# Kernel optimization log

Measured on AMD Instinct MI355X. Metric: run time of the kernel, lower is better.

## Reference

```python
import jax, jax.numpy as jnp
import numpy as np

MAX_DELAY = 128
INPUT = 64
HIDDEN = 128
HALF = HIDDEN // 2
OUT = 64
B = 32
T = 128
OUT_LEN = 64


def setup_inputs() -> dict:
    key = jax.random.key(0)
    ks = jax.random.split(key, 10)
    w = lambda k, sh: (jax.random.normal(k, sh, jnp.float32) * 0.05)
    return {
        "x": jax.random.normal(ks[0], (B, T, INPUT), jnp.float32),
        "lengths": jax.random.randint(ks[1], (B,), 0, T, jnp.int32),
        "out_lengths": OUT_LEN,
        "Wm": w(ks[2], (INPUT + HIDDEN, HIDDEN)), "bm": jnp.zeros((HIDDEN,), jnp.float32),
        "W1": w(ks[3], (HIDDEN, HALF)), "b1": jnp.zeros((HALF,), jnp.float32),
        "W2": w(ks[4], (HALF, 2 * HIDDEN)), "b2": jnp.zeros((2 * HIDDEN,), jnp.float32),
        "Wo": w(ks[5], (HIDDEN, OUT)), "bo": jnp.zeros((OUT,), jnp.float32),
    }


def reference(x, lengths, out_lengths, Wm, bm, W1, b1, W2, b2, Wo, bo):
    # index_tensor: (1, 1, max_delay) in [0, 1)
    index = (jnp.arange(MAX_DELAY, dtype=x.dtype) / MAX_DELAY)[None, None, :]

    def tau_gen(msg):  # msg: (B, H)
        h = jax.nn.relu(msg @ W1 + b1)
        tg = jax.nn.sigmoid(h @ W2 + b2)  # (B, 2H)
        return tg[:, :HIDDEN], tg[:, HIDDEN:]

    def update_buffer(buffer, msg, tau, mem_i):
        # shift left, zero-pad at the end
        new_buf = jnp.pad(buffer[:, :, 1:], ((0, 0), (0, 0), (0, 1)))
        iw = mem_i[..., None] * (1.0 - jnp.abs(tau[..., None] - index)) ** 2  # (B,H,D)
        return (1.0 - iw) * new_buf + iw * msg[..., None]

    masks = (jnp.arange(T) < lengths[:, None]).astype(x.dtype)  # (B, T)

    def enc_step(buffer, inp):
        x_t, mask = inp  # (B, I), (B,)
        m = mask[:, None]  # (B, 1)
        msg = m * jnp.tanh(jnp.concatenate([x_t, buffer[:, :, 0]], axis=-1) @ Wm + bm)
        tau, mem_i = tau_gen(msg)
        new_buf = update_buffer(buffer, msg, tau, mem_i)
        buffer = jnp.where(m[..., None] > 0, new_buf, buffer)
        return buffer, None

    buffer0 = jnp.zeros((B, HIDDEN, MAX_DELAY), x.dtype)
    buffer, _ = jax.lax.scan(enc_step, buffer0, (x.transpose(1, 0, 2), masks.T))

    x0 = jnp.zeros((B, INPUT), x.dtype)

    def dec_step(buffer, _):
        msg = jnp.tanh(jnp.concatenate([x0, buffer[:, :, 0]], axis=-1) @ Wm + bm)
        tau, mem_i = tau_gen(msg)
        buffer = update_buffer(buffer, msg, tau, mem_i)
        return buffer, msg @ Wo + bo

    _, outs = jax.lax.scan(dec_step, buffer, None, length=out_lengths)
    return outs.transpose(1, 0, 2)  # (B, out_lengths, OUT)
```

## Files before the change

kernel.cpp:

```cpp
#include <hip/hip_runtime.h>
#include <math.h>

typedef __attribute__((ext_vector_type(2))) float f32x2;

#define MAX_DELAY 128
#define INPUT 64
#define HIDDEN 128
#define HALF 64
#define OUT 64
#define BATCH 32
#define T 128
#define OUT_LEN 64
#define NTHR 512

static __device__ __forceinline__ f32x2 splat2(float v) { f32x2 r; r.x = v; r.y = v; return r; }

template <int CTRL>
static __device__ __forceinline__ float dpp_movf(float v) {
    return __int_as_float(__builtin_amdgcn_update_dpp(
        0, __float_as_int(v), CTRL, 0xF, 0xF, true));
}
#define DPP_XOR1 0xB1
#define DPP_XOR2 0x4E
#define DPP_ROT1 0x39
#define DPP_MIR8 0x141

__global__ __launch_bounds__(NTHR, 2)
void delayrnn_kernel(
    const float* __restrict__ x,
    const int*   __restrict__ lengths,
    const float* __restrict__ Wm,
    const float* __restrict__ bm,
    const float* __restrict__ W1,
    const float* __restrict__ b1,
    const float* __restrict__ W2,
    const float* __restrict__ b2,
    const float* __restrict__ Wo,
    const float* __restrict__ bo,
    float* __restrict__ out)
{
    const int b   = blockIdx.x;
    const int tid = threadIdx.x;
    const int len = lengths[b];
    const int total = len + OUT_LEN;

    const int h  = tid >> 2, q  = tid & 3;
    const int qq = q & 1,    qh = q >> 1;
    const int k1 = tid >> 3, r1 = tid & 7;
    const int co = tid >> 3, ro = tid & 7;

    f32x2 wm2[24];
#pragma unroll
    for (int j = 0; j < 24; ++j) {
        wm2[j].x = Wm[(q * 48 + 2 * j)     * HIDDEN + h];
        wm2[j].y = Wm[(q * 48 + 2 * j + 1) * HIDDEN + h];
    }
    f32x2 w12[8];
#pragma unroll
    for (int j = 0; j < 8; ++j) {
        w12[j].x = W1[(r1 * 16 + 2 * j)     * HALF + k1];
        w12[j].y = W1[(r1 * 16 + 2 * j + 1) * HALF + k1];
    }
    const int c2 = h + 128 * qh;
    f32x2 w22[16];
#pragma unroll
    for (int j = 0; j < 16; ++j) {
        w22[j].x = W2[(qq * 32 + 2 * j)     * (2 * HIDDEN) + c2];
        w22[j].y = W2[(qq * 32 + 2 * j + 1) * (2 * HIDDEN) + c2];
    }
    f32x2 wo2[8];
#pragma unroll
    for (int j = 0; j < 8; ++j) {
        wo2[j].x = Wo[(ro * 16 + 2 * j)     * OUT + co];
        wo2[j].y = Wo[(ro * 16 + 2 * j + 1) * OUT + co];
    }
    const float bm_r = bm[h];
    const float b1_r = b1[k1];
    const float b2_r = b2[c2];
    const float bo_r = bo[co];

    float buf[32];
#pragma unroll
    for (int d = 0; d < 32; ++d) buf[d] = 0.f;

    __shared__ float s_x[T * INPUT];
    __shared__ float s_v[INPUT + HIDDEN];
    __shared__ float s_msg[HIDDEN];
    __shared__ float s_h1[HALF];

    for (int idx = tid; idx < T * INPUT; idx += NTHR)
        s_x[idx] = x[b * T * INPUT + idx];
    if (tid < INPUT) s_v[tid] = (0 < len) ? x[b * T * INPUT + tid] : 0.f;
    if (tid >= INPUT && tid < INPUT + HIDDEN) s_v[tid] = 0.f;
    __syncthreads();

    const float ivb = (float)q * 0.25f;

    for (int i = 0; i < total; ++i) {
        const f32x2* v2 = (const f32x2*)(s_v + q * 48);
        f32x2 a0 = splat2(0.f), a1 = splat2(0.f), a2 = splat2(0.f), a3 = splat2(0.f);
#pragma unroll
        for (int j = 0; j < 24; j += 4) {
            a0 += wm2[j] * v2[j];         a1 += wm2[j + 1] * v2[j + 1];
            a2 += wm2[j + 2] * v2[j + 2]; a3 += wm2[j + 3] * v2[j + 3];
        }
        f32x2 aa = (a0 + a1) + (a2 + a3);
        float p = aa.x + aa.y;
        p += dpp_movf<DPP_XOR1>(p);
        p += dpp_movf<DPP_XOR2>(p);
        const float z  = p + bm_r;
        const float e2 = __expf(2.f * z);
        const float msg = 1.f - 2.f * __builtin_amdgcn_rcpf(e2 + 1.f);
        if (q == 0) s_msg[h] = msg;
        __syncthreads();

        const f32x2* m2 = (const f32x2*)(s_msg + r1 * 16);
        f32x2 c0 = splat2(0.f), c1 = splat2(0.f);
#pragma unroll
        for (int j = 0; j < 8; j += 2) { c0 += w12[j] * m2[j]; c1 += w12[j + 1] * m2[j + 1]; }
        f32x2 cc = c0 + c1;
        float p1 = cc.x + cc.y;
        p1 += dpp_movf<DPP_XOR1>(p1);
        p1 += dpp_movf<DPP_XOR2>(p1);
        p1 += dpp_movf<DPP_MIR8>(p1);
        if (r1 == 0) s_h1[k1] = fmaxf(p1 + b1_r, 0.f);
        __syncthreads();

        const f32x2* h2 = (const f32x2*)(s_h1 + qq * 32);
        f32x2 t0 = splat2(0.f), t1 = splat2(0.f);
#pragma unroll
        for (int j = 0; j < 16; j += 2) { t0 += w22[j] * h2[j]; t1 += w22[j + 1] * h2[j + 1]; }
        f32x2 tt = t0 + t1;
        float pt = tt.x + tt.y;
        pt += dpp_movf<DPP_XOR1>(pt);
        const float own = __builtin_amdgcn_rcpf(1.f + __expf(-(pt + b2_r)));
        const float oth = dpp_movf<DPP_XOR2>(own);
        const float tau_r = qh ? oth : own;
        const float mem_r = qh ? own : oth;

        {
            float tail_in = dpp_movf<DPP_ROT1>(buf[0]);
            if (q == 3) tail_in = 0.f;
            const float taup = tau_r - ivb;
            const f32x2 tau2 = splat2(taup);
            const f32x2 mem2 = splat2(mem_r);
            const f32x2 m2m  = splat2(-2.f * mem_r);
            const f32x2 msg2 = splat2(msg);
#pragma unroll
            for (int mp = 0; mp < 16; ++mp) {
                const int d = 2 * mp;
                f32x2 nb;
                nb.x = buf[d + 1];
                nb.y = (mp < 15) ? buf[d + 2] : tail_in;
                f32x2 t;
                t.x = tau2.x - (float)d       * (1.f / MAX_DELAY);
                t.y = tau2.y - (float)(d + 1) * (1.f / MAX_DELAY);
                f32x2 a  = __builtin_elementwise_max(t, -t);
                f32x2 f1 = a * mem2 + m2m;
                f32x2 iw = a * f1 + mem2;
                f32x2 dd = msg2 - nb;
                f32x2 nv = iw * dd + nb;
                buf[d] = nv.x; buf[d + 1] = nv.y;
            }
        }
        if (q == 0) s_v[INPUT + h] = buf[0];

        if (i >= len) {
            const f32x2* mo2 = (const f32x2*)(s_msg + ro * 16);
            f32x2 o0 = splat2(0.f), o1 = splat2(0.f);
#pragma unroll
            for (int j = 0; j < 8; j += 2) { o0 += wo2[j] * mo2[j]; o1 += wo2[j + 1] * mo2[j + 1]; }
            f32x2 oo = o0 + o1;
            float po = oo.x + oo.y;
            po += dpp_movf<DPP_XOR1>(po);
            po += dpp_movf<DPP_XOR2>(po);
            po += dpp_movf<DPP_MIR8>(po);
            if (ro == 0) out[(b * OUT_LEN + (i - len)) * OUT + co] = po + bo_r;
        }

        if (tid < INPUT) {
            const int nx = i + 1;
            s_v[tid] = (nx < len) ? s_x[nx * INPUT + tid] : 0.f;
        }
        __syncthreads();
    }
}

extern "C" void kernel_launch(void* const* d_in, const int* in_sizes, int n_in,
                              void* d_out, int out_size, void* d_ws, size_t ws_size,
                              hipStream_t stream) {
    const float* x       = (const float*)d_in[0];
    const int*   lengths = (const int*)  d_in[1];
    const float* Wm = (const float*)d_in[3];
    const float* bm = (const float*)d_in[4];
    const float* W1 = (const float*)d_in[5];
    const float* b1 = (const float*)d_in[6];
    const float* W2 = (const float*)d_in[7];
    const float* b2 = (const float*)d_in[8];
    const float* Wo = (const float*)d_in[9];
    const float* bo = (const float*)d_in[10];
    float* out = (float*)d_out;

    delayrnn_kernel<<<BATCH, NTHR, 0, stream>>>(
        x, lengths, Wm, bm, W1, b1, W2, b2, Wo, bo, out);
}
```

Baseline: 323.6 us.

## Defer buffer tail update to next step and hoist output projection off critical path

Only the head element buf[0], which feeds the next step's matvec, is updated right away. The remaining 31 buffer slots are updated lazily at the start of the next iteration using the saved msg, tau and mem. The output projection and the next-input staging are moved earlier, into the slots between barriers. This shortens the serial dependency chain between barriers so the bulk elementwise update can overlap with other work. The cost is extra live registers and a more subtle data flow, in particular the head_old rotation across lanes.

```diff
diff --git a/kernel.cpp b/kernel.cpp
--- a/kernel.cpp
+++ b/kernel.cpp
@@ -96,7 +96,37 @@
 
     const float ivb = (float)q * 0.25f;
 
+    float msg_p = 0.f, tau_p = 0.f, mem_p = 0.f, head_old = 0.f;
+
     for (int i = 0; i < total; ++i) {
+        {
+            float tail_in = dpp_movf<DPP_ROT1>(head_old);
+            if (q == 3) tail_in = 0.f;
+            const float taup = tau_p - ivb;
+            const f32x2 tau2 = splat2(taup);
+            const f32x2 mem2 = splat2(mem_p);
+            const f32x2 m2m  = splat2(-2.f * mem_p);
+            const f32x2 msg2 = splat2(msg_p);
+#pragma unroll
+            for (int mp = 0; mp < 15; ++mp) {
+                const int d = 2 * mp + 1;
+                f32x2 nb; nb.x = buf[d + 1]; nb.y = buf[d + 2];
+                f32x2 t;
+                t.x = tau2.x - (float)d       * (1.f / MAX_DELAY);
+                t.y = tau2.y - (float)(d + 1) * (1.f / MAX_DELAY);
+                f32x2 a  = __builtin_elementwise_max(t, -t);
+                f32x2 f1 = a * mem2 + m2m;
+                f32x2 iw = a * f1 + mem2;
+                f32x2 nv = iw * (msg2 - nb) + nb;
+                buf[d] = nv.x; buf[d + 1] = nv.y;
+            }
+            {
+                const float t31 = taup - 31.f * (1.f / MAX_DELAY);
+                const float a   = fabsf(t31);
+                const float iw  = a * (a * mem_p - 2.f * mem_p) + mem_p;
+                buf[31] = iw * (msg_p - tail_in) + tail_in;
+            }
+        }
         const f32x2* v2 = (const f32x2*)(s_v + q * 48);
         f32x2 a0 = splat2(0.f), a1 = splat2(0.f), a2 = splat2(0.f), a3 = splat2(0.f);
 #pragma unroll
@@ -108,8 +138,8 @@
         float p = aa.x + aa.y;
         p += dpp_movf<DPP_XOR1>(p);
         p += dpp_movf<DPP_XOR2>(p);
-        const float z  = p + bm_r;
-        const float e2 = __expf(2.f * z);
+        const float z   = p + bm_r;
+        const float e2  = __expf(2.f * z);
         const float msg = 1.f - 2.f * __builtin_amdgcn_rcpf(e2 + 1.f);
         if (q == 0) s_msg[h] = msg;
         __syncthreads();
@@ -124,12 +154,30 @@
         p1 += dpp_movf<DPP_XOR2>(p1);
         p1 += dpp_movf<DPP_MIR8>(p1);
         if (r1 == 0) s_h1[k1] = fmaxf(p1 + b1_r, 0.f);
+        if (tid < INPUT) {
+            const int nx = i + 1;
+            s_v[tid] = (nx < len) ? s_x[nx * INPUT + tid] : 0.f;
+        }
         __syncthreads();
 
         const f32x2* h2 = (const f32x2*)(s_h1 + qq * 32);
         f32x2 t0 = splat2(0.f), t1 = splat2(0.f);
 #pragma unroll
         for (int j = 0; j < 16; j += 2) { t0 += w22[j] * h2[j]; t1 += w22[j + 1] * h2[j + 1]; }
+
+        if (i >= len) {
+            const f32x2* mo2 = (const f32x2*)(s_msg + ro * 16);
+            f32x2 o0 = splat2(0.f), o1 = splat2(0.f);
+#pragma unroll
+            for (int j = 0; j < 8; j += 2) { o0 += wo2[j] * mo2[j]; o1 += wo2[j + 1] * mo2[j + 1]; }
+            f32x2 oo = o0 + o1;
+            float po = oo.x + oo.y;
+            po += dpp_movf<DPP_XOR1>(po);
+            po += dpp_movf<DPP_XOR2>(po);
+            po += dpp_movf<DPP_MIR8>(po);
+            if (ro == 0) out[(b * OUT_LEN + (i - len)) * OUT + co] = po + bo_r;
+        }
+
         f32x2 tt = t0 + t1;
         float pt = tt.x + tt.y;
         pt += dpp_movf<DPP_XOR1>(pt);
@@ -138,50 +186,17 @@
         const float tau_r = qh ? oth : own;
         const float mem_r = qh ? own : oth;
 
+        head_old = buf[0];
         {
-            float tail_in = dpp_movf<DPP_ROT1>(buf[0]);
-            if (q == 3) tail_in = 0.f;
-            const float taup = tau_r - ivb;
-            const f32x2 tau2 = splat2(taup);
-            const f32x2 mem2 = splat2(mem_r);
-            const f32x2 m2m  = splat2(-2.f * mem_r);
-            const f32x2 msg2 = splat2(msg);
-#pragma unroll
-            for (int mp = 0; mp < 16; ++mp) {
-                const int d = 2 * mp;
-                f32x2 nb;
-                nb.x = buf[d + 1];
-                nb.y = (mp < 15) ? buf[d + 2] : tail_in;
-                f32x2 t;
-                t.x = tau2.x - (float)d       * (1.f / MAX_DELAY);
-                t.y = tau2.y - (float)(d + 1) * (1.f / MAX_DELAY);
-                f32x2 a  = __builtin_elementwise_max(t, -t);
-                f32x2 f1 = a * mem2 + m2m;
-                f32x2 iw = a * f1 + mem2;
-                f32x2 dd = msg2 - nb;
-                f32x2 nv = iw * dd + nb;
-                buf[d] = nv.x; buf[d + 1] = nv.y;
-            }
+            const float t0h = tau_r - ivb;
+            const float a   = fabsf(t0h);
+            const float iw  = a * (a * mem_r - 2.f * mem_r) + mem_r;
+            const float nb  = buf[1];
+            buf[0] = iw * (msg - nb) + nb;
         }
         if (q == 0) s_v[INPUT + h] = buf[0];
 
-        if (i >= len) {
-            const f32x2* mo2 = (const f32x2*)(s_msg + ro * 16);
-            f32x2 o0 = splat2(0.f), o1 = splat2(0.f);
-#pragma unroll
-            for (int j = 0; j < 8; j += 2) { o0 += wo2[j] * mo2[j]; o1 += wo2[j + 1] * mo2[j + 1]; }
-            f32x2 oo = o0 + o1;
-            float po = oo.x + oo.y;
-            po += dpp_movf<DPP_XOR1>(po);
-            po += dpp_movf<DPP_XOR2>(po);
-            po += dpp_movf<DPP_MIR8>(po);
-            if (ro == 0) out[(b * OUT_LEN + (i - len)) * OUT + co] = po + bo_r;
-        }
-
-        if (tid < INPUT) {
-            const int nx = i + 1;
-            s_v[tid] = (nx < len) ? s_x[nx * INPUT + tid] : 0.f;
-        }
+        msg_p = msg; tau_p = tau_r; mem_p = mem_r;
         __syncthreads();
     }
 }
```

After: 325.7 us. About the same (+0.6%).

## Split block into compute and buffer-update warp groups with one-step lagged pipeline

Applied to the files above, without the earlier changes.

Threads are split into two halves. The first 256 threads run the matvec chain (Wm, W1, W2, Wo) and compute buffer[:,:,0] for the next step directly from a staged y1 value. The other 256 threads hold the 128-wide delay buffer in registers and apply the blend one step behind, spread across the barrier phases. This takes the full buffer update off the critical path of the recurrence, and the Wo projection is deferred by one step and overlapped with the W1 stage. In exchange each thread holds more registers (48+16+32+16 f32x2 weights or 64 buffer floats) and the loop has an extra barrier per step.

```diff
diff --git a/kernel.cpp b/kernel.cpp
--- a/kernel.cpp
+++ b/kernel.cpp
@@ -22,8 +22,6 @@
 }
 #define DPP_XOR1 0xB1
 #define DPP_XOR2 0x4E
-#define DPP_ROT1 0x39
-#define DPP_MIR8 0x141
 
 __global__ __launch_bounds__(NTHR, 2)
 void delayrnn_kernel(
@@ -44,145 +42,191 @@
     const int len = lengths[b];
     const int total = len + OUT_LEN;
 
-    const int h  = tid >> 2, q  = tid & 3;
-    const int qq = q & 1,    qh = q >> 1;
-    const int k1 = tid >> 3, r1 = tid & 7;
-    const int co = tid >> 3, ro = tid & 7;
-
-    f32x2 wm2[24];
-#pragma unroll
-    for (int j = 0; j < 24; ++j) {
-        wm2[j].x = Wm[(q * 48 + 2 * j)     * HIDDEN + h];
-        wm2[j].y = Wm[(q * 48 + 2 * j + 1) * HIDDEN + h];
-    }
-    f32x2 w12[8];
-#pragma unroll
-    for (int j = 0; j < 8; ++j) {
-        w12[j].x = W1[(r1 * 16 + 2 * j)     * HALF + k1];
-        w12[j].y = W1[(r1 * 16 + 2 * j + 1) * HALF + k1];
-    }
-    const int c2 = h + 128 * qh;
-    f32x2 w22[16];
-#pragma unroll
-    for (int j = 0; j < 16; ++j) {
-        w22[j].x = W2[(qq * 32 + 2 * j)     * (2 * HIDDEN) + c2];
-        w22[j].y = W2[(qq * 32 + 2 * j + 1) * (2 * HIDDEN) + c2];
-    }
-    f32x2 wo2[8];
-#pragma unroll
-    for (int j = 0; j < 8; ++j) {
-        wo2[j].x = Wo[(ro * 16 + 2 * j)     * OUT + co];
-        wo2[j].y = Wo[(ro * 16 + 2 * j + 1) * OUT + co];
-    }
-    const float bm_r = bm[h];
-    const float b1_r = b1[k1];
-    const float b2_r = b2[c2];
-    const float bo_r = bo[co];
-
-    float buf[32];
-#pragma unroll
-    for (int d = 0; d < 32; ++d) buf[d] = 0.f;
-
     __shared__ float s_x[T * INPUT];
     __shared__ float s_v[INPUT + HIDDEN];
-    __shared__ float s_msg[HIDDEN];
+    __shared__ float s_msg[2][HIDDEN];
     __shared__ float s_h1[HALF];
+    __shared__ float s_tau[HIDDEN];
+    __shared__ float s_mem[HIDDEN];
+    __shared__ float s_y1[HIDDEN];
 
     for (int idx = tid; idx < T * INPUT; idx += NTHR)
         s_x[idx] = x[b * T * INPUT + idx];
     if (tid < INPUT) s_v[tid] = (0 < len) ? x[b * T * INPUT + tid] : 0.f;
     if (tid >= INPUT && tid < INPUT + HIDDEN) s_v[tid] = 0.f;
+    if (tid < HIDDEN) { s_y1[tid] = 0.f; s_tau[tid] = 0.f; s_mem[tid] = 0.f; }
     __syncthreads();
 
-    const float ivb = (float)q * 0.25f;
-
-    for (int i = 0; i < total; ++i) {
-        const f32x2* v2 = (const f32x2*)(s_v + q * 48);
-        f32x2 a0 = splat2(0.f), a1 = splat2(0.f), a2 = splat2(0.f), a3 = splat2(0.f);
-#pragma unroll
-        for (int j = 0; j < 24; j += 4) {
-            a0 += wm2[j] * v2[j];         a1 += wm2[j + 1] * v2[j + 1];
-            a2 += wm2[j + 2] * v2[j + 2]; a3 += wm2[j + 3] * v2[j + 3];
-        }
-        f32x2 aa = (a0 + a1) + (a2 + a3);
-        float p = aa.x + aa.y;
-        p += dpp_movf<DPP_XOR1>(p);
-        p += dpp_movf<DPP_XOR2>(p);
-        const float z  = p + bm_r;
-        const float e2 = __expf(2.f * z);
-        const float msg = 1.f - 2.f * __builtin_amdgcn_rcpf(e2 + 1.f);
-        if (q == 0) s_msg[h] = msg;
-        __syncthreads();
-
-        const f32x2* m2 = (const f32x2*)(s_msg + r1 * 16);
-        f32x2 c0 = splat2(0.f), c1 = splat2(0.f);
-#pragma unroll
-        for (int j = 0; j < 8; j += 2) { c0 += w12[j] * m2[j]; c1 += w12[j + 1] * m2[j + 1]; }
-        f32x2 cc = c0 + c1;
-        float p1 = cc.x + cc.y;
-        p1 += dpp_movf<DPP_XOR1>(p1);
-        p1 += dpp_movf<DPP_XOR2>(p1);
-        p1 += dpp_movf<DPP_MIR8>(p1);
-        if (r1 == 0) s_h1[k1] = fmaxf(p1 + b1_r, 0.f);
-        __syncthreads();
-
-        const f32x2* h2 = (const f32x2*)(s_h1 + qq * 32);
-        f32x2 t0 = splat2(0.f), t1 = splat2(0.f);
-#pragma unroll
-        for (int j = 0; j < 16; j += 2) { t0 += w22[j] * h2[j]; t1 += w22[j + 1] * h2[j + 1]; }
-        f32x2 tt = t0 + t1;
-        float pt = tt.x + tt.y;
-        pt += dpp_movf<DPP_XOR1>(pt);
-        const float own = __builtin_amdgcn_rcpf(1.f + __expf(-(pt + b2_r)));
-        const float oth = dpp_movf<DPP_XOR2>(own);
-        const float tau_r = qh ? oth : own;
-        const float mem_r = qh ? own : oth;
+    if (tid < 256) {
+        const int ch = tid >> 1, r   = tid & 1;
+        const int k1 = tid >> 2, r4  = tid & 3;
+        const int cl = tid;
+        const int oc = tid >> 2, orr = tid & 3;
+
+        f32x2 wm[48];
+#pragma unroll
+        for (int j = 0; j < 48; ++j) {
+            wm[j].x = Wm[(r * 96 + 2 * j)     * HIDDEN + ch];
+            wm[j].y = Wm[(r * 96 + 2 * j + 1) * HIDDEN + ch];
+        }
+        f32x2 w1[16];
+#pragma unroll
+        for (int j = 0; j < 16; ++j) {
+            w1[j].x = W1[(r4 * 32 + 2 * j)     * HALF + k1];
+            w1[j].y = W1[(r4 * 32 + 2 * j + 1) * HALF + k1];
+        }
+        f32x2 w2[32];
+#pragma unroll
+        for (int j = 0; j < 32; ++j) {
+            w2[j].x = W2[(2 * j)     * (2 * HIDDEN) + cl];
+            w2[j].y = W2[(2 * j + 1) * (2 * HIDDEN) + cl];
+        }
+        f32x2 wo[16];
+#pragma unroll
+        for (int j = 0; j < 16; ++j) {
+            wo[j].x = Wo[(orr * 32 + 2 * j)     * OUT + oc];
+            wo[j].y = Wo[(orr * 32 + 2 * j + 1) * OUT + oc];
+        }
+        const float bm_r = bm[ch];
+        const float b1_r = b1[k1];
+        const float b2_r = b2[cl];
+        const float bo_r = bo[oc];
+
+        float tau_own = 0.f;
+
+        for (int i = 0; i < total; ++i) {
+            const int par = i & 1;
+            const f32x2* v2 = (const f32x2*)(s_v + r * 96);
+            f32x2 a0 = splat2(0.f), a1 = splat2(0.f), a2 = splat2(0.f), a3 = splat2(0.f);
+#pragma unroll
+            for (int j = 0; j < 48; j += 4) {
+                a0 += wm[j] * v2[j];         a1 += wm[j + 1] * v2[j + 1];
+                a2 += wm[j + 2] * v2[j + 2]; a3 += wm[j + 3] * v2[j + 3];
+            }
+            f32x2 aa = (a0 + a1) + (a2 + a3);
+            float p = aa.x + aa.y;
+            p += dpp_movf<DPP_XOR1>(p);
+            const float z   = p + bm_r;
+            const float e2  = __expf(2.f * z);
+            const float msg = 1.f - 2.f * __builtin_amdgcn_rcpf(e2 + 1.f);
+            if (r == 0) s_msg[par][ch] = msg;
+            __syncthreads();
+
+            const f32x2* m2 = (const f32x2*)(s_msg[par] + r4 * 32);
+            f32x2 c0 = splat2(0.f), c1 = splat2(0.f);
+#pragma unroll
+            for (int j = 0; j < 16; j += 2) { c0 += w1[j] * m2[j]; c1 += w1[j + 1] * m2[j + 1]; }
+            f32x2 cc = c0 + c1;
+            float p1 = cc.x + cc.y;
+            p1 += dpp_movf<DPP_XOR1>(p1);
+            p1 += dpp_movf<DPP_XOR2>(p1);
+            if (r4 == 0) s_h1[k1] = fmaxf(p1 + b1_r, 0.f);
+            if (i - 1 >= len) {
+                const f32x2* mo = (const f32x2*)(s_msg[par ^ 1] + orr * 32);
+                f32x2 o0 = splat2(0.f), o1 = splat2(0.f);
+#pragma unroll
+                for (int j = 0; j < 16; j += 2) { o0 += wo[j] * mo[j]; o1 += wo[j + 1] * mo[j + 1]; }
+                f32x2 oo = o0 + o1;
+                float po = oo.x + oo.y;
+                po += dpp_movf<DPP_XOR1>(po);
+                po += dpp_movf<DPP_XOR2>(po);
+                if (orr == 0) out[(b * OUT_LEN + (i - 1 - len)) * OUT + oc] = po + bo_r;
+            }
+            __syncthreads();
+
+            const f32x2* h2 = (const f32x2*)s_h1;
+            f32x2 t0 = splat2(0.f), t1 = splat2(0.f);
+#pragma unroll
+            for (int j = 0; j < 32; j += 2) { t0 += w2[j] * h2[j]; t1 += w2[j + 1] * h2[j + 1]; }
+            f32x2 tt = t0 + t1;
+            const float pt = tt.x + tt.y;
+            const float g = __builtin_amdgcn_rcpf(1.f + __expf(-(pt + b2_r)));
+            if (cl < HIDDEN) { s_tau[cl] = g; tau_own = g; }
+            else             s_mem[cl - HIDDEN] = g;
+            __syncthreads();
+
+            if (cl < HIDDEN) {
+                const float msg_i = s_msg[par][cl];
+                const float mem_i = s_mem[cl];
+                const float nb    = s_y1[cl];
+                const float a     = fabsf(tau_own);
+                const float iw    = a * (a * mem_i - 2.f * mem_i) + mem_i;
+                s_v[INPUT + cl] = nb + iw * (msg_i - nb);
+            }
+            if (tid < INPUT) {
+                const int nx = i + 1;
+                s_v[tid] = (nx < len) ? s_x[nx * INPUT + tid] : 0.f;
+            }
+            __syncthreads();
+        }
 
         {
-            float tail_in = dpp_movf<DPP_ROT1>(buf[0]);
-            if (q == 3) tail_in = 0.f;
-            const float taup = tau_r - ivb;
-            const f32x2 tau2 = splat2(taup);
-            const f32x2 mem2 = splat2(mem_r);
-            const f32x2 m2m  = splat2(-2.f * mem_r);
-            const f32x2 msg2 = splat2(msg);
-#pragma unroll
-            for (int mp = 0; mp < 16; ++mp) {
-                const int d = 2 * mp;
-                f32x2 nb;
-                nb.x = buf[d + 1];
-                nb.y = (mp < 15) ? buf[d + 2] : tail_in;
-                f32x2 t;
-                t.x = tau2.x - (float)d       * (1.f / MAX_DELAY);
-                t.y = tau2.y - (float)(d + 1) * (1.f / MAX_DELAY);
-                f32x2 a  = __builtin_elementwise_max(t, -t);
-                f32x2 f1 = a * mem2 + m2m;
-                f32x2 iw = a * f1 + mem2;
-                f32x2 dd = msg2 - nb;
-                f32x2 nv = iw * dd + nb;
-                buf[d] = nv.x; buf[d + 1] = nv.y;
-            }
-        }
-        if (q == 0) s_v[INPUT + h] = buf[0];
-
-        if (i >= len) {
-            const f32x2* mo2 = (const f32x2*)(s_msg + ro * 16);
+            const int par = (total - 1) & 1;
+            const f32x2* mo = (const f32x2*)(s_msg[par] + orr * 32);
             f32x2 o0 = splat2(0.f), o1 = splat2(0.f);
 #pragma unroll
-            for (int j = 0; j < 8; j += 2) { o0 += wo2[j] * mo2[j]; o1 += wo2[j + 1] * mo2[j + 1]; }
+            for (int j = 0; j < 16; j += 2) { o0 += wo[j] * mo[j]; o1 += wo[j + 1] * mo[j + 1]; }
             f32x2 oo = o0 + o1;
             float po = oo.x + oo.y;
             po += dpp_movf<DPP_XOR1>(po);
             po += dpp_movf<DPP_XOR2>(po);
-            po += dpp_movf<DPP_MIR8>(po);
-            if (ro == 0) out[(b * OUT_LEN + (i - len)) * OUT + co] = po + bo_r;
-        }
-
-        if (tid < INPUT) {
-            const int nx = i + 1;
-            s_v[tid] = (nx < len) ? s_x[nx * INPUT + tid] : 0.f;
-        }
-        __syncthreads();
+            if (orr == 0) out[(b * OUT_LEN + (OUT_LEN - 1)) * OUT + oc] = po + bo_r;
+        }
+    } else {
+        const int v  = tid - 256;
+        const int ch = v >> 1, pp = v & 1;
+        float buf[64];
+#pragma unroll
+        for (int d = 0; d < 64; ++d) buf[d] = 0.f;
+
+        const float ivb = pp ? 0.5f : 0.f;
+        float msg_p = 0.f, tau_p = 0.f, mem_p = 0.f;
+
+        for (int i = 0; i < total; ++i) {
+            const int par = i & 1;
+            const float old64 = dpp_movf<DPP_XOR1>(buf[0]);
+            const float taup  = tau_p - ivb;
+            const f32x2 tau2  = splat2(taup);
+            const f32x2 mem2  = splat2(mem_p);
+            const f32x2 m2m   = splat2(-2.f * mem_p);
+            const f32x2 msg2  = splat2(msg_p);
+            const float tail  = pp ? 0.f : old64;
+
+#define BLEND_PAIR(M)                                                        \
+            {                                                                \
+                const int k = 2 * (M);                                       \
+                f32x2 nb;                                                    \
+                nb.x = buf[k + 1];                                           \
+                nb.y = ((M) < 31) ? buf[k + 2] : tail;                       \
+                f32x2 t;                                                     \
+                t.x = tau2.x - (float)k       * (1.f / MAX_DELAY);           \
+                t.y = tau2.y - (float)(k + 1) * (1.f / MAX_DELAY);           \
+                f32x2 a  = __builtin_elementwise_max(t, -t);                 \
+                f32x2 f1 = a * mem2 + m2m;                                   \
+                f32x2 iw = a * f1 + mem2;                                    \
+                f32x2 nv = iw * (msg2 - nb) + nb;                            \
+                buf[k] = nv.x; buf[k + 1] = nv.y;                            \
+            }
+
+#pragma unroll
+            for (int m = 0; m <= 10; ++m) BLEND_PAIR(m)
+            if (pp == 0) s_y1[ch] = buf[1];
+            __syncthreads();
+
+#pragma unroll
+            for (int m = 11; m <= 21; ++m) BLEND_PAIR(m)
+            __syncthreads();
+
+#pragma unroll
+            for (int m = 22; m <= 31; ++m) BLEND_PAIR(m)
+            __syncthreads();
+
+            msg_p = s_msg[par][ch];
+            tau_p = s_tau[ch];
+            mem_p = s_mem[ch];
+            __syncthreads();
+#undef BLEND_PAIR
+        }
     }
 }
 
```

New measurement: 447.3 us. 38.2% more time.
